# Kernel tuning notes

Measured on AMD Instinct MI355X. Metric: run time of the kernel, lower is better.

Reference implementation:

```python
import jax, jax.numpy as jnp
import numpy as np

N_NODES = 100000
N_EDGES = 1600000
N_GRAPHS = 2048


def _gcn_conv(x, src, dst, W, b, n_nodes):
    # PyG GCNConv: add self-loops, symmetric norm D^-1/2 A D^-1/2, then linear.
    h = x @ W  # [N, H]
    loop = jnp.arange(n_nodes, dtype=src.dtype)
    s = jnp.concatenate([src, loop])
    d = jnp.concatenate([dst, loop])
    deg = jax.ops.segment_sum(jnp.ones_like(d, dtype=h.dtype), d, num_segments=n_nodes)
    dinv = jax.lax.rsqrt(jnp.maximum(deg, 1.0))
    norm = dinv[s] * dinv[d]  # [E+N]
    msg = h[s] * norm[:, None]  # gathered, normalized messages
    out = jax.ops.segment_sum(msg, d, num_segments=n_nodes)
    return out + b


def _mean_pool(x, batch, n_graphs):
    sums = jax.ops.segment_sum(x, batch, num_segments=n_graphs)
    cnt = jax.ops.segment_sum(jnp.ones((x.shape[0],), x.dtype), batch, num_segments=n_graphs)
    return sums / jnp.maximum(cnt, 1.0)[:, None]


def setup_inputs() -> dict:
    key = jax.random.key(0)
    ks = jax.random.split(key, 8)
    x = jax.random.normal(ks[0], (N_NODES, 128), dtype=jnp.float32)
    edge_index = jax.random.randint(ks[1], (2, N_EDGES), 0, N_NODES, dtype=jnp.int64)
    batch = jnp.sort(jax.random.randint(ks[2], (N_NODES,), 0, N_GRAPHS, dtype=jnp.int64))
    W1 = jax.random.normal(ks[3], (128, 256), dtype=jnp.float32) * 0.05
    b1 = jnp.zeros((256,), jnp.float32)
    W2 = jax.random.normal(ks[4], (256, 256), dtype=jnp.float32) * 0.05
    b2 = jnp.zeros((256,), jnp.float32)
    Wc = jax.random.normal(ks[5], (256, 64), dtype=jnp.float32) * 0.05
    bc = jnp.zeros((64,), jnp.float32)
    return {"x": x, "edge_index": edge_index, "batch": batch,
            "W1": W1, "b1": b1, "W2": W2, "b2": b2, "Wc": Wc, "bc": bc}


def reference(x, edge_index, batch, W1, b1, W2, b2, Wc, bc):
    src, dst = edge_index[0], edge_index[1]
    n = x.shape[0]
    h = jax.nn.relu(_gcn_conv(x, src, dst, W1, b1, n))
    h = jax.nn.relu(_gcn_conv(h, src, dst, W2, b2, n))
    g = _mean_pool(h, batch, N_GRAPHS)  # [G, h2]
    logits = g @ Wc + bc
    return jax.nn.log_softmax(logits, axis=1)
```

## Files before the change

kernel.cpp:

```cpp
#include <hip/hip_runtime.h>
#include <hip/hip_bf16.h>

#define N_NODES 100000
#define N_EDGES 1600000
#define N_GRAPHS 2048
#define F0 128
#define F1 256
#define NCLS 64

#define BSHIFT 9
#define BNODES 512
#define NB 196
#define EPB 4096
#define NCHUNK 391
#define FLATN (NB * NCHUNK)

typedef unsigned int uint32;
typedef unsigned short u16;
typedef u16 u16x8 __attribute__((ext_vector_type(8)));
typedef __bf16 bf16x8 __attribute__((ext_vector_type(8)));
typedef float f32x4 __attribute__((ext_vector_type(4)));

__device__ __forceinline__ float blo(uint32 v) { return __builtin_bit_cast(float, v << 16); }
__device__ __forceinline__ float bhi(uint32 v) { return __builtin_bit_cast(float, v & 0xffff0000u); }
__device__ __forceinline__ float b16f(u16 v) { return __builtin_bit_cast(float, (uint32)v << 16); }
__device__ __forceinline__ u16 f2bf(float f) {
    uint32 u = __builtin_bit_cast(uint32, f);
    u += 0x7fffu + ((u >> 16) & 1u);
    return (u16)(u >> 16);
}
__device__ __forceinline__ uint32 pack2(float a, float b) {
    return (uint32)f2bf(a) | ((uint32)f2bf(b) << 16);
}

#define SCAN_B 1024

__global__ void scan_partial(const int* __restrict__ in, int n, int* __restrict__ bsum) {
    __shared__ int lds[SCAN_B];
    int i = blockIdx.x * SCAN_B + threadIdx.x;
    lds[threadIdx.x] = (i < n) ? in[i] : 0;
    __syncthreads();
    for (int s = SCAN_B / 2; s > 0; s >>= 1) {
        if (threadIdx.x < s) lds[threadIdx.x] += lds[threadIdx.x + s];
        __syncthreads();
    }
    if (threadIdx.x == 0) bsum[blockIdx.x] = lds[0];
}

__global__ void scan_bsum(int* __restrict__ bsum, int nb) {
    __shared__ int lds[SCAN_B];
    int v = (threadIdx.x < nb) ? bsum[threadIdx.x] : 0;
    lds[threadIdx.x] = v;
    __syncthreads();
    for (int s = 1; s < SCAN_B; s <<= 1) {
        int t = (threadIdx.x >= s) ? lds[threadIdx.x - s] : 0;
        __syncthreads();
        lds[threadIdx.x] += t;
        __syncthreads();
    }
    if (threadIdx.x < nb) bsum[threadIdx.x] = lds[threadIdx.x] - v;
}

__global__ void scan_final(const int* __restrict__ in, int n, const int* __restrict__ bsum,
                           int* __restrict__ out) {
    __shared__ int lds[SCAN_B];
    int i = blockIdx.x * SCAN_B + threadIdx.x;
    int v = (i < n) ? in[i] : 0;
    lds[threadIdx.x] = v;
    __syncthreads();
    for (int s = 1; s < SCAN_B; s <<= 1) {
        int t = (threadIdx.x >= s) ? lds[threadIdx.x - s] : 0;
        __syncthreads();
        lds[threadIdx.x] += t;
        __syncthreads();
    }
    if (i < n) out[i + 1] = lds[threadIdx.x] + bsum[blockIdx.x];
    if (i == 0) out[0] = 0;
}


__global__ __launch_bounds__(256) void hist_pass(const int* __restrict__ dst,
                                                 int* __restrict__ hist) {
    __shared__ int lh[NB];
    int t = threadIdx.x, blk = blockIdx.x;
    if (t < NB) lh[t] = 0;
    __syncthreads();
#pragma unroll
    for (int k = 0; k < EPB / 256; ++k) {
        int e = blk * EPB + k * 256 + t;
        if (e < N_EDGES) atomicAdd(&lh[dst[e] >> BSHIFT], 1);
    }
    __syncthreads();
    if (t < NB) hist[t * NCHUNK + blk] = lh[t];
}

__global__ __launch_bounds__(256) void bin_pairs(const int* __restrict__ src,
                                                 const int* __restrict__ dst,
                                                 const int* __restrict__ histoff,
                                                 uint32* __restrict__ pairs) {
    __shared__ int lbase[NB];
    __shared__ int lcur[NB];
    int t = threadIdx.x, blk = blockIdx.x;
    if (t < NB) {
        lbase[t] = histoff[t * NCHUNK + blk];
        lcur[t] = 0;
    }
    __syncthreads();
#pragma unroll
    for (int k = 0; k < EPB / 256; ++k) {
        int e = blk * EPB + k * 256 + t;
        if (e < N_EDGES) {
            int d = dst[e], s = src[e];
            int b = d >> BSHIFT;
            int r = atomicAdd(&lcur[b], 1);
            pairs[lbase[b] + r] = (uint32)(d & (BNODES - 1)) | ((uint32)s << BSHIFT);
        }
    }
}

__global__ __launch_bounds__(256) void bucket_csr(const uint32* __restrict__ pairs,
                                                  const int* __restrict__ histoff,
                                                  int* __restrict__ offs,
                                                  int* __restrict__ csr,
                                                  float* __restrict__ dinv) {
    __shared__ int lcnt[BNODES];
    __shared__ int lcur[BNODES];
    __shared__ int psum[256];
    int t = threadIdx.x, b = blockIdx.x;
    int n0 = b << BSHIFT;
    int nn = min(BNODES, N_NODES - n0);
    lcnt[t] = 0;
    lcnt[t + 256] = 0;
    __syncthreads();
    int ebase = histoff[b * NCHUNK];
    int eend = (b == NB - 1) ? N_EDGES : histoff[(b + 1) * NCHUNK];
    for (int i = ebase + t; i < eend; i += 256) {
        atomicAdd(&lcnt[pairs[i] & (BNODES - 1)], 1);
    }
    __syncthreads();
    int c0 = lcnt[2 * t], c1 = lcnt[2 * t + 1];
    if (2 * t < nn) dinv[n0 + 2 * t] = rsqrtf((float)(c0 + 1));
    if (2 * t + 1 < nn) dinv[n0 + 2 * t + 1] = rsqrtf((float)(c1 + 1));
    psum[t] = c0 + c1;
    __syncthreads();
    for (int s = 1; s < 256; s <<= 1) {
        int v = (t >= s) ? psum[t - s] : 0;
        __syncthreads();
        psum[t] += v;
        __syncthreads();
    }
    int ep = psum[t] - (c0 + c1);
    lcur[2 * t] = ep;
    lcur[2 * t + 1] = ep + c0;
    if (2 * t < nn) offs[n0 + 2 * t] = ebase + ep;
    if (2 * t + 1 < nn) offs[n0 + 2 * t + 1] = ebase + ep + c0;
    if (b == NB - 1 && t == 0) offs[N_NODES] = N_EDGES;
    __syncthreads();
    for (int i = ebase + t; i < eend; i += 256) {
        uint32 p = pairs[i];
        int r = atomicAdd(&lcur[p & (BNODES - 1)], 1);
        csr[ebase + r] = (int)(p >> BSHIFT);
    }
}


__global__ __launch_bounds__(256) void cast_q8_x(const float* __restrict__ x,
                                                 const float* __restrict__ dinv,
                                                 const int* __restrict__ batch,
                                                 u16* __restrict__ q8,
                                                 float* __restrict__ qs,
                                                 int* __restrict__ gcnt) {
    int node = blockIdx.x * 4 + (threadIdx.x >> 6);
    if (node >= N_NODES) return;
    int lane = threadIdx.x & 63;
    float d = dinv[node];
    float2 v = *(const float2*)&x[(size_t)node * F0 + lane * 2];
    float f0 = v.x * d, f1 = v.y * d;
    float m = fmaxf(fabsf(f0), fabsf(f1));
    for (int s = 32; s > 0; s >>= 1) m = fmaxf(m, __shfl_xor(m, s, 64));
    float inv = (m > 0.f) ? 127.f / m : 0.f;
    int q0 = (int)rintf(f0 * inv), q1 = (int)rintf(f1 * inv);
    q8[(size_t)node * 64 + lane] = (u16)((q0 & 255) | ((q1 & 255) << 8));
    if (lane == 0) {
        qs[node] = m * (1.f / 127.f);
        atomicAdd(&gcnt[batch[node]], 1);
    }
}


__global__ __launch_bounds__(256) void quantize_rows(const u16* __restrict__ hs1,
                                                     uint32* __restrict__ q8,
                                                     float* __restrict__ qs) {
    int node = blockIdx.x * 4 + (threadIdx.x >> 6);
    if (node >= N_NODES) return;
    int lane = threadIdx.x & 63;
    uint2 v = *(const uint2*)&hs1[(size_t)node * F1 + lane * 4];
    float f0 = blo(v.x), f1 = bhi(v.x), f2 = blo(v.y), f3 = bhi(v.y);
    float m = fmaxf(fmaxf(f0, f1), fmaxf(f2, f3));
    for (int s = 32; s > 0; s >>= 1) m = fmaxf(m, __shfl_xor(m, s, 64));
    float inv = (m > 0.f) ? 127.f / m : 0.f;
    int q0 = (int)rintf(f0 * inv), q1 = (int)rintf(f1 * inv);
    int q2 = (int)rintf(f2 * inv), q3 = (int)rintf(f3 * inv);
    q8[(size_t)node * 64 + lane] =
        (uint32)(q0 & 255) | ((uint32)(q1 & 255) << 8) | ((uint32)(q2 & 255) << 16) | ((uint32)q3 << 24);
    if (lane == 0) qs[node] = m * (1.f / 127.f);
}


__global__ void transpose_w2(const float* __restrict__ W1, const float* __restrict__ W2,
                             u16* __restrict__ W1t, u16* __restrict__ W2t) {
    int id = blockIdx.x * blockDim.x + threadIdx.x;
    if (id < F0 * F1) {
        int k = id / F1, n = id % F1;
        W1t[(size_t)n * F0 + k] = f2bf(W1[id]);
    } else {
        int id2 = id - F0 * F1;
        if (id2 < F1 * F1) {
            int k = id2 / F1, n = id2 % F1;
            W2t[(size_t)n * F1 + k] = f2bf(W2[id2]);
        }
    }
}


template <int F>
__global__ __launch_bounds__(256) void aggregate_q8(const void* __restrict__ q8,
                                                    const float* __restrict__ qs,
                                                    const int* __restrict__ offs,
                                                    const int* __restrict__ csr,
                                                    const float* __restrict__ dinv,
                                                    u16* __restrict__ out) {
    constexpr int V = F / 64;
    int node = blockIdx.x * 4 + (threadIdx.x >> 6);
    if (node >= N_NODES) return;
    int lane = threadIdx.x & 63;
    float acc[V];
    {
        float s = qs[node];
        if constexpr (V == 2) {
            int q = (int)((const u16*)q8)[(size_t)node * 64 + lane];
            acc[0] = (float)((q << 24) >> 24) * s;
            acc[1] = (float)((q << 16) >> 24) * s;
        } else {
            int q = (int)((const uint32*)q8)[(size_t)node * 64 + lane];
            acc[0] = (float)((q << 24) >> 24) * s;
            acc[1] = (float)((q << 16) >> 24) * s;
            acc[2] = (float)((q << 8) >> 24) * s;
            acc[3] = (float)(q >> 24) * s;
        }
    }
    int e0 = offs[node], e1 = offs[node + 1];
    for (int b = e0; b < e1; b += 64) {
        bool valid = (b + lane) < e1;
        int idx = valid ? csr[b + lane] : 0;
        float sv = valid ? qs[idx] : 0.f;
        int cnt = min(64, e1 - b);
        int t = 0;
        for (; t + 4 <= cnt; t += 4) {
            int j0 = __shfl(idx, t), j1 = __shfl(idx, t + 1);
            int j2 = __shfl(idx, t + 2), j3 = __shfl(idx, t + 3);
            float s0 = __shfl(sv, t), s1 = __shfl(sv, t + 1);
            float s2 = __shfl(sv, t + 2), s3 = __shfl(sv, t + 3);
            if constexpr (V == 2) {
                int a = (int)((const u16*)q8)[(size_t)j0 * 64 + lane];
                int c = (int)((const u16*)q8)[(size_t)j1 * 64 + lane];
                int d = (int)((const u16*)q8)[(size_t)j2 * 64 + lane];
                int f = (int)((const u16*)q8)[(size_t)j3 * 64 + lane];
                acc[0] += (float)((a << 24) >> 24) * s0 + (float)((c << 24) >> 24) * s1 +
                          (float)((d << 24) >> 24) * s2 + (float)((f << 24) >> 24) * s3;
                acc[1] += (float)((a << 16) >> 24) * s0 + (float)((c << 16) >> 24) * s1 +
                          (float)((d << 16) >> 24) * s2 + (float)((f << 16) >> 24) * s3;
            } else {
                int a = (int)((const uint32*)q8)[(size_t)j0 * 64 + lane];
                int c = (int)((const uint32*)q8)[(size_t)j1 * 64 + lane];
                int d = (int)((const uint32*)q8)[(size_t)j2 * 64 + lane];
                int f = (int)((const uint32*)q8)[(size_t)j3 * 64 + lane];
                acc[0] += (float)((a << 24) >> 24) * s0 + (float)((c << 24) >> 24) * s1 +
                          (float)((d << 24) >> 24) * s2 + (float)((f << 24) >> 24) * s3;
                acc[1] += (float)((a << 16) >> 24) * s0 + (float)((c << 16) >> 24) * s1 +
                          (float)((d << 16) >> 24) * s2 + (float)((f << 16) >> 24) * s3;
                acc[2] += (float)((a << 8) >> 24) * s0 + (float)((c << 8) >> 24) * s1 +
                          (float)((d << 8) >> 24) * s2 + (float)((f << 8) >> 24) * s3;
                acc[3] += (float)(a >> 24) * s0 + (float)(c >> 24) * s1 +
                          (float)(d >> 24) * s2 + (float)(f >> 24) * s3;
            }
        }
        for (; t < cnt; ++t) {
            int j0 = __shfl(idx, t);
            float s0 = __shfl(sv, t);
            if constexpr (V == 2) {
                int a = (int)((const u16*)q8)[(size_t)j0 * 64 + lane];
                acc[0] += (float)((a << 24) >> 24) * s0;
                acc[1] += (float)((a << 16) >> 24) * s0;
            } else {
                int a = (int)((const uint32*)q8)[(size_t)j0 * 64 + lane];
                acc[0] += (float)((a << 24) >> 24) * s0;
                acc[1] += (float)((a << 16) >> 24) * s0;
                acc[2] += (float)((a << 8) >> 24) * s0;
                acc[3] += (float)(a >> 24) * s0;
            }
        }
    }
    float di = dinv[node];
    u16* orow = out + (size_t)node * F + lane * V;
    if constexpr (V == 2) {
        *(uint32*)orow = pack2(acc[0] * di, acc[1] * di);
    } else {
        uint2 o;
        o.x = pack2(acc[0] * di, acc[1] * di);
        o.y = pack2(acc[2] * di, acc[3] * di);
        *(uint2*)orow = o;
    }
}


template <int K, bool SCALE, bool POOL>
__global__ __launch_bounds__(256) void gemm_mfma(const u16* __restrict__ A,
                                                 const u16* __restrict__ Bt,
                                                 const float* __restrict__ bias,
                                                 const float* __restrict__ dinv,
                                                 u16* __restrict__ C, int M,
                                                 const int* __restrict__ batch,
                                                 float* __restrict__ gpool) {
    constexpr int BM = 128, BN = 128, BK = 64, BKP = 72;
    constexpr int NN = 256;
    __shared__ __align__(16) char smem[2 * BM * BKP * 2];
    u16(*As)[BKP] = (u16(*)[BKP])smem;
    u16(*Bs)[BKP] = (u16(*)[BKP])(smem + BM * BKP * 2);
    int tid = threadIdx.x;
    int row0 = blockIdx.x * BM, col0 = blockIdx.y * BN;
    int lane = tid & 63, wid = tid >> 6;
    int wm = (wid >> 1) * 64, wn = (wid & 1) * 64;
    int lr = lane & 15, lq = lane >> 4;

    f32x4 acc[4][4];
#pragma unroll
    for (int i = 0; i < 4; ++i)
#pragma unroll
        for (int j = 0; j < 4; ++j) acc[i][j] = (f32x4){0.f, 0.f, 0.f, 0.f};

    for (int k0 = 0; k0 < K; k0 += BK) {
#pragma unroll
        for (int p = 0; p < 4; ++p) {
            int r = (tid >> 3) + p * 32;
            int c = (tid & 7) * 8;
            u16x8 av = {0, 0, 0, 0, 0, 0, 0, 0};
            int gr = row0 + r;
            if (gr < M) av = *(const u16x8*)&A[(size_t)gr * K + k0 + c];
            *(u16x8*)&As[r][c] = av;
            *(u16x8*)&Bs[r][c] = *(const u16x8*)&Bt[(size_t)(col0 + r) * K + k0 + c];
        }
        __syncthreads();
#pragma unroll
        for (int kk = 0; kk < BK; kk += 32) {
            bf16x8 af[4], bfr[4];
#pragma unroll
            for (int i = 0; i < 4; ++i)
                af[i] = __builtin_bit_cast(bf16x8, *(const u16x8*)&As[wm + i * 16 + lr][kk + lq * 8]);
#pragma unroll
            for (int j = 0; j < 4; ++j)
                bfr[j] = __builtin_bit_cast(bf16x8, *(const u16x8*)&Bs[wn + j * 16 + lr][kk + lq * 8]);
#pragma unroll
            for (int i = 0; i < 4; ++i)
#pragma unroll
                for (int j = 0; j < 4; ++j)
                    acc[i][j] = __builtin_amdgcn_mfma_f32_16x16x32_bf16(af[i], bfr[j], acc[i][j], 0, 0, 0);
        }
        __syncthreads();
    }

    if constexpr (!POOL) {
#pragma unroll
        for (int i = 0; i < 4; ++i) {
#pragma unroll
            for (int j = 0; j < 4; ++j) {
                int col = col0 + wn + j * 16 + lr;
                float bv = bias[col];
#pragma unroll
                for (int r = 0; r < 4; ++r) {
                    int row = row0 + wm + i * 16 + lq * 4 + r;
                    if (row < M) {
                        float v = fmaxf(acc[i][j][r] + bv, 0.f);
                        if constexpr (SCALE) v *= dinv[row];
                        C[(size_t)row * NN + col] = f2bf(v);
                    }
                }
            }
        }
    } else {
        u16(*P)[130] = (u16(*)[130])smem;
        int* batchl = (int*)(smem + 33280);
#pragma unroll
        for (int i = 0; i < 4; ++i) {
#pragma unroll
            for (int j = 0; j < 4; ++j) {
                int cl = wn + j * 16 + lr;
                float bv = bias[col0 + cl];
#pragma unroll
                for (int r = 0; r < 4; ++r) {
                    int rl = wm + i * 16 + lq * 4 + r;
                    float v = (row0 + rl < M) ? fmaxf(acc[i][j][r] + bv, 0.f) : 0.f;
                    P[rl][cl] = f2bf(v);
                }
            }
        }
        if (tid < BM) {
            int row = row0 + tid;
            batchl[tid] = batch[row < M ? row : (M - 1)];
        }
        __syncthreads();
        int c = tid & 127;
        int h = tid >> 7;
        int cur = batchl[h * 64];
        float sum = 0.f;
#pragma unroll 4
        for (int r = h * 64; r < h * 64 + 64; ++r) {
            int gb = batchl[r];
            float v = b16f(P[r][c]);
            if (gb != cur) {
                atomicAdd(&gpool[(size_t)cur * NN + col0 + c], sum);
                sum = 0.f;
                cur = gb;
            }
            sum += v;
        }
        atomicAdd(&gpool[(size_t)cur * NN + col0 + c], sum);
    }
}


__global__ void classify(const float* __restrict__ gpool, const int* __restrict__ gcnt,
                         const float* __restrict__ Wc, const float* __restrict__ bc,
                         float* __restrict__ out) {
    int gr = blockIdx.x;
    int c = threadIdx.x;
    __shared__ float gl[F1];
    float inv = 1.f / fmaxf((float)gcnt[gr], 1.f);
    for (int k = c; k < F1; k += 64) gl[k] = gpool[(size_t)gr * F1 + k] * inv;
    __syncthreads();
    float acc = bc[c];
    for (int k = 0; k < F1; ++k) acc += gl[k] * Wc[k * NCLS + c];
    float m = acc;
    for (int s = 32; s > 0; s >>= 1) m = fmaxf(m, __shfl_xor(m, s, 64));
    float ex = __expf(acc - m);
    float sum = ex;
    for (int s = 32; s > 0; s >>= 1) sum += __shfl_xor(sum, s, 64);
    out[(size_t)gr * NCLS + c] = acc - m - __logf(sum);
}


extern "C" void kernel_launch(void* const* d_in, const int* in_sizes, int n_in,
                              void* d_out, int out_size, void* d_ws, size_t ws_size,
                              hipStream_t stream) {
    const float* x = (const float*)d_in[0];
    const int* ei = (const int*)d_in[1];
    const int* batch = (const int*)d_in[2];
    const float* W1 = (const float*)d_in[3];
    const float* b1 = (const float*)d_in[4];
    const float* W2 = (const float*)d_in[5];
    const float* b2 = (const float*)d_in[6];
    const float* Wc = (const float*)d_in[7];
    const float* bc = (const float*)d_in[8];
    float* out = (float*)d_out;
    const int* src = ei;
    const int* dst = ei + N_EDGES;

    char* w = (char*)d_ws;
    auto take = [&](size_t n) { char* p = w; w += (n + 255) & ~(size_t)255; return p; };
    float* dinv = (float*)take((size_t)N_NODES * 4);
    int* offs = (int*)take((size_t)(N_NODES + 1) * 4);
    int* hist = (int*)take((size_t)FLATN * 4);
    int* histoff = (int*)take((size_t)(FLATN + 1) * 4);
    int* bsum = (int*)take((size_t)1024 * 4);
    int* gcnt = (int*)take((size_t)N_GRAPHS * 4);
    uint32* pairs = (uint32*)take((size_t)N_EDGES * 4);
    int* csr = (int*)take((size_t)N_EDGES * 4);
    u16* q8x = (u16*)take((size_t)N_NODES * 64 * 2);
    float* qsx = (float*)take((size_t)N_NODES * 4);
    uint32* q8h = (uint32*)take((size_t)N_NODES * 64 * 4);
    float* qsh = (float*)take((size_t)N_NODES * 4);
    u16* aggx = (u16*)take((size_t)N_NODES * F0 * 2);
    u16* hs1 = (u16*)take((size_t)N_NODES * F1 * 2);
    u16* agg1 = (u16*)take((size_t)N_NODES * F1 * 2);
    u16* W1t = (u16*)take((size_t)F0 * F1 * 2);
    u16* W2t = (u16*)take((size_t)F1 * F1 * 2);
    float* gpool = (float*)take((size_t)N_GRAPHS * F1 * 4);

    hipMemsetAsync(gcnt, 0, (size_t)N_GRAPHS * 4, stream);
    hipMemsetAsync(gpool, 0, (size_t)N_GRAPHS * F1 * 4, stream);

    hist_pass<<<NCHUNK, 256, 0, stream>>>(dst, hist);
    {
        int nb = (FLATN + SCAN_B - 1) / SCAN_B;
        scan_partial<<<nb, SCAN_B, 0, stream>>>(hist, FLATN, bsum);
        scan_bsum<<<1, SCAN_B, 0, stream>>>(bsum, nb);
        scan_final<<<nb, SCAN_B, 0, stream>>>(hist, FLATN, bsum, histoff);
    }
    bin_pairs<<<NCHUNK, 256, 0, stream>>>(src, dst, histoff, pairs);
    bucket_csr<<<NB, 256, 0, stream>>>(pairs, histoff, offs, csr, dinv);

    transpose_w2<<<(F0 * F1 + F1 * F1 + 255) / 256, 256, 0, stream>>>(W1, W2, W1t, W2t);
    cast_q8_x<<<(N_NODES + 3) / 4, 256, 0, stream>>>(x, dinv, batch, q8x, qsx, gcnt);

    aggregate_q8<F0><<<(N_NODES + 3) / 4, 256, 0, stream>>>(q8x, qsx, offs, csr, dinv, aggx);
    gemm_mfma<F0, true, false><<<dim3((N_NODES + 127) / 128, 2), 256, 0, stream>>>(
        aggx, W1t, b1, dinv, hs1, N_NODES, nullptr, nullptr);

    quantize_rows<<<(N_NODES + 3) / 4, 256, 0, stream>>>(hs1, q8h, qsh);

    aggregate_q8<F1><<<(N_NODES + 3) / 4, 256, 0, stream>>>(q8h, qsh, offs, csr, dinv, agg1);
    gemm_mfma<F1, false, true><<<dim3((N_NODES + 127) / 128, 2), 256, 0, stream>>>(
        agg1, W2t, b2, dinv, nullptr, N_NODES, batch, gpool);

    classify<<<N_GRAPHS, 64, 0, stream>>>(gpool, gcnt, Wc, bc, out);
}
```

Baseline: 464.9 us.

## Fuse row quantization into GEMM epilogue with full-width tiles and offset-binary int8

The GEMM tile changes to 64x256 so each block covers a full output row. The first layer's GEMM can then compute per-row max and quantize to int8 directly from shared memory, which removes the separate quantize_rows kernel and the bf16 hs1 round trip through global memory. Quantized values are now stored as unsigned offset-binary (+128), and the aggregation removes the offset with a running scale sum, which simplifies byte extraction to unsigned conversions. The smaller M tile reloads the full B matrix per block and lengthens the serial pooling loop per thread. The epilogue also needs extra LDS passes and barriers.

```diff
diff --git a/kernel.cpp b/kernel.cpp
--- a/kernel.cpp
+++ b/kernel.cpp
@@ -32,6 +32,10 @@
 __device__ __forceinline__ uint32 pack2(float a, float b) {
     return (uint32)f2bf(a) | ((uint32)f2bf(b) << 16);
 }
+__device__ __forceinline__ float ub0(uint32 u) { return (float)(u & 255u); }
+__device__ __forceinline__ float ub1(uint32 u) { return (float)((u >> 8) & 255u); }
+__device__ __forceinline__ float ub2(uint32 u) { return (float)((u >> 16) & 255u); }
+__device__ __forceinline__ float ub3(uint32 u) { return (float)(u >> 24); }
 
 #define SCAN_B 1024
 
@@ -179,31 +183,12 @@
     float m = fmaxf(fabsf(f0), fabsf(f1));
     for (int s = 32; s > 0; s >>= 1) m = fmaxf(m, __shfl_xor(m, s, 64));
     float inv = (m > 0.f) ? 127.f / m : 0.f;
-    int q0 = (int)rintf(f0 * inv), q1 = (int)rintf(f1 * inv);
-    q8[(size_t)node * 64 + lane] = (u16)((q0 & 255) | ((q1 & 255) << 8));
+    int u0 = (int)rintf(f0 * inv) + 128, u1 = (int)rintf(f1 * inv) + 128;
+    q8[(size_t)node * 64 + lane] = (u16)((u0 & 255) | ((u1 & 255) << 8));
     if (lane == 0) {
         qs[node] = m * (1.f / 127.f);
         atomicAdd(&gcnt[batch[node]], 1);
     }
-}
-
-
-__global__ __launch_bounds__(256) void quantize_rows(const u16* __restrict__ hs1,
-                                                     uint32* __restrict__ q8,
-                                                     float* __restrict__ qs) {
-    int node = blockIdx.x * 4 + (threadIdx.x >> 6);
-    if (node >= N_NODES) return;
-    int lane = threadIdx.x & 63;
-    uint2 v = *(const uint2*)&hs1[(size_t)node * F1 + lane * 4];
-    float f0 = blo(v.x), f1 = bhi(v.x), f2 = blo(v.y), f3 = bhi(v.y);
-    float m = fmaxf(fmaxf(f0, f1), fmaxf(f2, f3));
-    for (int s = 32; s > 0; s >>= 1) m = fmaxf(m, __shfl_xor(m, s, 64));
-    float inv = (m > 0.f) ? 127.f / m : 0.f;
-    int q0 = (int)rintf(f0 * inv), q1 = (int)rintf(f1 * inv);
-    int q2 = (int)rintf(f2 * inv), q3 = (int)rintf(f3 * inv);
-    q8[(size_t)node * 64 + lane] =
-        (uint32)(q0 & 255) | ((uint32)(q1 & 255) << 8) | ((uint32)(q2 & 255) << 16) | ((uint32)q3 << 24);
-    if (lane == 0) qs[node] = m * (1.f / 127.f);
 }
 
 
@@ -235,18 +220,20 @@
     if (node >= N_NODES) return;
     int lane = threadIdx.x & 63;
     float acc[V];
+    float ssum;
     {
         float s = qs[node];
+        ssum = s;
         if constexpr (V == 2) {
-            int q = (int)((const u16*)q8)[(size_t)node * 64 + lane];
-            acc[0] = (float)((q << 24) >> 24) * s;
-            acc[1] = (float)((q << 16) >> 24) * s;
+            uint32 q = (uint32)((const u16*)q8)[(size_t)node * 64 + lane];
+            acc[0] = ub0(q) * s;
+            acc[1] = ub1(q) * s;
         } else {
-            int q = (int)((const uint32*)q8)[(size_t)node * 64 + lane];
-            acc[0] = (float)((q << 24) >> 24) * s;
-            acc[1] = (float)((q << 16) >> 24) * s;
-            acc[2] = (float)((q << 8) >> 24) * s;
-            acc[3] = (float)(q >> 24) * s;
+            uint32 q = ((const uint32*)q8)[(size_t)node * 64 + lane];
+            acc[0] = ub0(q) * s;
+            acc[1] = ub1(q) * s;
+            acc[2] = ub2(q) * s;
+            acc[3] = ub3(q) * s;
         }
     }
     int e0 = offs[node], e1 = offs[node + 1];
@@ -261,76 +248,74 @@
             int j2 = __shfl(idx, t + 2), j3 = __shfl(idx, t + 3);
             float s0 = __shfl(sv, t), s1 = __shfl(sv, t + 1);
             float s2 = __shfl(sv, t + 2), s3 = __shfl(sv, t + 3);
+            ssum += (s0 + s1) + (s2 + s3);
             if constexpr (V == 2) {
-                int a = (int)((const u16*)q8)[(size_t)j0 * 64 + lane];
-                int c = (int)((const u16*)q8)[(size_t)j1 * 64 + lane];
-                int d = (int)((const u16*)q8)[(size_t)j2 * 64 + lane];
-                int f = (int)((const u16*)q8)[(size_t)j3 * 64 + lane];
-                acc[0] += (float)((a << 24) >> 24) * s0 + (float)((c << 24) >> 24) * s1 +
-                          (float)((d << 24) >> 24) * s2 + (float)((f << 24) >> 24) * s3;
-                acc[1] += (float)((a << 16) >> 24) * s0 + (float)((c << 16) >> 24) * s1 +
-                          (float)((d << 16) >> 24) * s2 + (float)((f << 16) >> 24) * s3;
+                uint32 a = (uint32)((const u16*)q8)[(size_t)j0 * 64 + lane];
+                uint32 c = (uint32)((const u16*)q8)[(size_t)j1 * 64 + lane];
+                uint32 d = (uint32)((const u16*)q8)[(size_t)j2 * 64 + lane];
+                uint32 f = (uint32)((const u16*)q8)[(size_t)j3 * 64 + lane];
+                acc[0] += ub0(a) * s0 + ub0(c) * s1 + ub0(d) * s2 + ub0(f) * s3;
+                acc[1] += ub1(a) * s0 + ub1(c) * s1 + ub1(d) * s2 + ub1(f) * s3;
             } else {
-                int a = (int)((const uint32*)q8)[(size_t)j0 * 64 + lane];
-                int c = (int)((const uint32*)q8)[(size_t)j1 * 64 + lane];
-                int d = (int)((const uint32*)q8)[(size_t)j2 * 64 + lane];
-                int f = (int)((const uint32*)q8)[(size_t)j3 * 64 + lane];
-                acc[0] += (float)((a << 24) >> 24) * s0 + (float)((c << 24) >> 24) * s1 +
-                          (float)((d << 24) >> 24) * s2 + (float)((f << 24) >> 24) * s3;
-                acc[1] += (float)((a << 16) >> 24) * s0 + (float)((c << 16) >> 24) * s1 +
-                          (float)((d << 16) >> 24) * s2 + (float)((f << 16) >> 24) * s3;
-                acc[2] += (float)((a << 8) >> 24) * s0 + (float)((c << 8) >> 24) * s1 +
-                          (float)((d << 8) >> 24) * s2 + (float)((f << 8) >> 24) * s3;
-                acc[3] += (float)(a >> 24) * s0 + (float)(c >> 24) * s1 +
-                          (float)(d >> 24) * s2 + (float)(f >> 24) * s3;
+                uint32 a = ((const uint32*)q8)[(size_t)j0 * 64 + lane];
+                uint32 c = ((const uint32*)q8)[(size_t)j1 * 64 + lane];
+                uint32 d = ((const uint32*)q8)[(size_t)j2 * 64 + lane];
+                uint32 f = ((const uint32*)q8)[(size_t)j3 * 64 + lane];
+                acc[0] += ub0(a) * s0 + ub0(c) * s1 + ub0(d) * s2 + ub0(f) * s3;
+                acc[1] += ub1(a) * s0 + ub1(c) * s1 + ub1(d) * s2 + ub1(f) * s3;
+                acc[2] += ub2(a) * s0 + ub2(c) * s1 + ub2(d) * s2 + ub2(f) * s3;
+                acc[3] += ub3(a) * s0 + ub3(c) * s1 + ub3(d) * s2 + ub3(f) * s3;
             }
         }
         for (; t < cnt; ++t) {
             int j0 = __shfl(idx, t);
             float s0 = __shfl(sv, t);
+            ssum += s0;
             if constexpr (V == 2) {
-                int a = (int)((const u16*)q8)[(size_t)j0 * 64 + lane];
-                acc[0] += (float)((a << 24) >> 24) * s0;
-                acc[1] += (float)((a << 16) >> 24) * s0;
+                uint32 a = (uint32)((const u16*)q8)[(size_t)j0 * 64 + lane];
+                acc[0] += ub0(a) * s0;
+                acc[1] += ub1(a) * s0;
             } else {
-                int a = (int)((const uint32*)q8)[(size_t)j0 * 64 + lane];
-                acc[0] += (float)((a << 24) >> 24) * s0;
-                acc[1] += (float)((a << 16) >> 24) * s0;
-                acc[2] += (float)((a << 8) >> 24) * s0;
-                acc[3] += (float)(a >> 24) * s0;
+                uint32 a = ((const uint32*)q8)[(size_t)j0 * 64 + lane];
+                acc[0] += ub0(a) * s0;
+                acc[1] += ub1(a) * s0;
+                acc[2] += ub2(a) * s0;
+                acc[3] += ub3(a) * s0;
             }
         }
     }
     float di = dinv[node];
+    float bias = 128.f * ssum;
     u16* orow = out + (size_t)node * F + lane * V;
     if constexpr (V == 2) {
-        *(uint32*)orow = pack2(acc[0] * di, acc[1] * di);
+        *(uint32*)orow = pack2((acc[0] - bias) * di, (acc[1] - bias) * di);
     } else {
         uint2 o;
-        o.x = pack2(acc[0] * di, acc[1] * di);
-        o.y = pack2(acc[2] * di, acc[3] * di);
+        o.x = pack2((acc[0] - bias) * di, (acc[1] - bias) * di);
+        o.y = pack2((acc[2] - bias) * di, (acc[3] - bias) * di);
         *(uint2*)orow = o;
     }
 }
 
 
-template <int K, bool SCALE, bool POOL>
-__global__ __launch_bounds__(256) void gemm_mfma(const u16* __restrict__ A,
-                                                 const u16* __restrict__ Bt,
-                                                 const float* __restrict__ bias,
-                                                 const float* __restrict__ dinv,
-                                                 u16* __restrict__ C, int M,
-                                                 const int* __restrict__ batch,
-                                                 float* __restrict__ gpool) {
-    constexpr int BM = 128, BN = 128, BK = 64, BKP = 72;
-    constexpr int NN = 256;
-    __shared__ __align__(16) char smem[2 * BM * BKP * 2];
+template <int K, bool QUANT>
+__global__ __launch_bounds__(256) void gemm_fused(const u16* __restrict__ A,
+                                                  const u16* __restrict__ Bt,
+                                                  const float* __restrict__ bias,
+                                                  const float* __restrict__ dinv,
+                                                  int M,
+                                                  uint32* __restrict__ q8,
+                                                  float* __restrict__ qs,
+                                                  const int* __restrict__ batch,
+                                                  float* __restrict__ gpool) {
+    constexpr int BM = 64, BN = 256, BK = 64, BKP = 72;
+    __shared__ __align__(16) char smem[46080];
     u16(*As)[BKP] = (u16(*)[BKP])smem;
     u16(*Bs)[BKP] = (u16(*)[BKP])(smem + BM * BKP * 2);
     int tid = threadIdx.x;
-    int row0 = blockIdx.x * BM, col0 = blockIdx.y * BN;
+    int row0 = blockIdx.x * BM;
     int lane = tid & 63, wid = tid >> 6;
-    int wm = (wid >> 1) * 64, wn = (wid & 1) * 64;
+    int wn = wid * 64;
     int lr = lane & 15, lq = lane >> 4;
 
     f32x4 acc[4][4];
@@ -340,15 +325,19 @@
         for (int j = 0; j < 4; ++j) acc[i][j] = (f32x4){0.f, 0.f, 0.f, 0.f};
 
     for (int k0 = 0; k0 < K; k0 += BK) {
-#pragma unroll
-        for (int p = 0; p < 4; ++p) {
+        int c = (tid & 7) * 8;
+#pragma unroll
+        for (int p = 0; p < 2; ++p) {
             int r = (tid >> 3) + p * 32;
-            int c = (tid & 7) * 8;
             u16x8 av = {0, 0, 0, 0, 0, 0, 0, 0};
             int gr = row0 + r;
             if (gr < M) av = *(const u16x8*)&A[(size_t)gr * K + k0 + c];
             *(u16x8*)&As[r][c] = av;
-            *(u16x8*)&Bs[r][c] = *(const u16x8*)&Bt[(size_t)(col0 + r) * K + k0 + c];
+        }
+#pragma unroll
+        for (int p = 0; p < 8; ++p) {
+            int r = (tid >> 3) + p * 32;
+            *(u16x8*)&Bs[r][c] = *(const u16x8*)&Bt[(size_t)r * K + k0 + c];
         }
         __syncthreads();
 #pragma unroll
@@ -356,7 +345,7 @@
             bf16x8 af[4], bfr[4];
 #pragma unroll
             for (int i = 0; i < 4; ++i)
-                af[i] = __builtin_bit_cast(bf16x8, *(const u16x8*)&As[wm + i * 16 + lr][kk + lq * 8]);
+                af[i] = __builtin_bit_cast(bf16x8, *(const u16x8*)&As[i * 16 + lr][kk + lq * 8]);
 #pragma unroll
             for (int j = 0; j < 4; ++j)
                 bfr[j] = __builtin_bit_cast(bf16x8, *(const u16x8*)&Bs[wn + j * 16 + lr][kk + lq * 8]);
@@ -369,62 +358,78 @@
         __syncthreads();
     }
 
-    if constexpr (!POOL) {
-#pragma unroll
-        for (int i = 0; i < 4; ++i) {
-#pragma unroll
-            for (int j = 0; j < 4; ++j) {
-                int col = col0 + wn + j * 16 + lr;
-                float bv = bias[col];
-#pragma unroll
-                for (int r = 0; r < 4; ++r) {
-                    int row = row0 + wm + i * 16 + lq * 4 + r;
-                    if (row < M) {
-                        float v = fmaxf(acc[i][j][r] + bv, 0.f);
-                        if constexpr (SCALE) v *= dinv[row];
-                        C[(size_t)row * NN + col] = f2bf(v);
-                    }
+    u16(*P)[260] = (u16(*)[260])smem;
+#pragma unroll
+    for (int i = 0; i < 4; ++i) {
+#pragma unroll
+        for (int j = 0; j < 4; ++j) {
+            int cl = wn + j * 16 + lr;
+            float bv = bias[cl];
+#pragma unroll
+            for (int r = 0; r < 4; ++r) {
+                int rl = i * 16 + lq * 4 + r;
+                int row = row0 + rl;
+                float v = 0.f;
+                if (row < M) {
+                    v = fmaxf(acc[i][j][r] + bv, 0.f);
+                    if constexpr (QUANT) v *= dinv[row];
                 }
+                P[rl][cl] = f2bf(v);
             }
         }
+    }
+
+    if constexpr (QUANT) {
+        float* rmax = (float*)(smem + 33280);
+        __syncthreads();
+        int row = tid & 63, q = tid >> 6;
+        float m = 0.f;
+#pragma unroll 8
+        for (int i = 0; i < 64; ++i) m = fmaxf(m, b16f(P[row][q * 64 + i]));
+        rmax[q * 64 + row] = m;
+        __syncthreads();
+        m = fmaxf(fmaxf(rmax[row], rmax[64 + row]), fmaxf(rmax[128 + row], rmax[192 + row]));
+        int gr = row0 + row;
+        if (gr < M) {
+            float inv = (m > 0.f) ? 127.f / m : 0.f;
+#pragma unroll
+            for (int d = 0; d < 16; d += 4) {
+                uint32 dw[4];
+#pragma unroll
+                for (int e = 0; e < 4; ++e) {
+                    int cb = q * 64 + (d + e) * 4;
+                    uint32 v0 = (uint32)((int)rintf(b16f(P[row][cb + 0]) * inv) + 128);
+                    uint32 v1 = (uint32)((int)rintf(b16f(P[row][cb + 1]) * inv) + 128);
+                    uint32 v2 = (uint32)((int)rintf(b16f(P[row][cb + 2]) * inv) + 128);
+                    uint32 v3 = (uint32)((int)rintf(b16f(P[row][cb + 3]) * inv) + 128);
+                    dw[e] = v0 | (v1 << 8) | (v2 << 16) | (v3 << 24);
+                }
+                *(uint4*)&q8[(size_t)gr * 64 + q * 16 + d] = make_uint4(dw[0], dw[1], dw[2], dw[3]);
+            }
+            if (q == 0) qs[gr] = m * (1.f / 127.f);
+        }
     } else {
-        u16(*P)[130] = (u16(*)[130])smem;
         int* batchl = (int*)(smem + 33280);
-#pragma unroll
-        for (int i = 0; i < 4; ++i) {
-#pragma unroll
-            for (int j = 0; j < 4; ++j) {
-                int cl = wn + j * 16 + lr;
-                float bv = bias[col0 + cl];
-#pragma unroll
-                for (int r = 0; r < 4; ++r) {
-                    int rl = wm + i * 16 + lq * 4 + r;
-                    float v = (row0 + rl < M) ? fmaxf(acc[i][j][r] + bv, 0.f) : 0.f;
-                    P[rl][cl] = f2bf(v);
-                }
-            }
-        }
         if (tid < BM) {
             int row = row0 + tid;
             batchl[tid] = batch[row < M ? row : (M - 1)];
         }
         __syncthreads();
-        int c = tid & 127;
-        int h = tid >> 7;
-        int cur = batchl[h * 64];
+        int c = tid;
+        int nrows = min(BM, M - row0);
+        int cur = batchl[0];
         float sum = 0.f;
-#pragma unroll 4
-        for (int r = h * 64; r < h * 64 + 64; ++r) {
+        for (int r = 0; r < nrows; ++r) {
             int gb = batchl[r];
             float v = b16f(P[r][c]);
             if (gb != cur) {
-                atomicAdd(&gpool[(size_t)cur * NN + col0 + c], sum);
+                atomicAdd(&gpool[(size_t)cur * BN + c], sum);
                 sum = 0.f;
                 cur = gb;
             }
             sum += v;
         }
-        atomicAdd(&gpool[(size_t)cur * NN + col0 + c], sum);
+        atomicAdd(&gpool[(size_t)cur * BN + c], sum);
     }
 }
 
@@ -480,7 +485,6 @@
     uint32* q8h = (uint32*)take((size_t)N_NODES * 64 * 4);
     float* qsh = (float*)take((size_t)N_NODES * 4);
     u16* aggx = (u16*)take((size_t)N_NODES * F0 * 2);
-    u16* hs1 = (u16*)take((size_t)N_NODES * F1 * 2);
     u16* agg1 = (u16*)take((size_t)N_NODES * F1 * 2);
     u16* W1t = (u16*)take((size_t)F0 * F1 * 2);
     u16* W2t = (u16*)take((size_t)F1 * F1 * 2);
@@ -502,15 +506,15 @@
     transpose_w2<<<(F0 * F1 + F1 * F1 + 255) / 256, 256, 0, stream>>>(W1, W2, W1t, W2t);
     cast_q8_x<<<(N_NODES + 3) / 4, 256, 0, stream>>>(x, dinv, batch, q8x, qsx, gcnt);
 
+    int mblocks = (N_NODES + 63) / 64;
+
     aggregate_q8<F0><<<(N_NODES + 3) / 4, 256, 0, stream>>>(q8x, qsx, offs, csr, dinv, aggx);
-    gemm_mfma<F0, true, false><<<dim3((N_NODES + 127) / 128, 2), 256, 0, stream>>>(
-        aggx, W1t, b1, dinv, hs1, N_NODES, nullptr, nullptr);
-
-    quantize_rows<<<(N_NODES + 3) / 4, 256, 0, stream>>>(hs1, q8h, qsh);
+    gemm_fused<F0, true><<<mblocks, 256, 0, stream>>>(aggx, W1t, b1, dinv, N_NODES,
+                                                      q8h, qsh, nullptr, nullptr);
 
     aggregate_q8<F1><<<(N_NODES + 3) / 4, 256, 0, stream>>>(q8h, qsh, offs, csr, dinv, agg1);
-    gemm_mfma<F1, false, true><<<dim3((N_NODES + 127) / 128, 2), 256, 0, stream>>>(
-        agg1, W2t, b2, dinv, nullptr, N_NODES, batch, gpool);
+    gemm_fused<F1, false><<<mblocks, 256, 0, stream>>>(agg1, W2t, b2, dinv, N_NODES,
+                                                       nullptr, nullptr, batch, gpool);
 
     classify<<<N_GRAPHS, 64, 0, stream>>>(gpool, gcnt, Wc, bc, out);
 }
```

New measurement: 460.4 us. Within noise of the previous version (-1.0%).
